# Kernel optimization log

Hardware: AMD Instinct MI355X
Metric: run time of the kernel (lower is better)

The kernel has to match this reference:

```python
import jax, jax.numpy as jnp
import numpy as np

B, T, D = 32, 4096, 256
P, K, L = 2, 17, 3
NH, HD, FF, HID = 8, 32, 2048, 128


def _ln(x, w, b):
    m = x.mean(-1, keepdims=True)
    v = ((x - m) ** 2).mean(-1, keepdims=True)
    return (x - m) * jax.lax.rsqrt(v + 1e-5) * w + b


def _refine(x, w1, b1, w2, b2):
    # x: (B,P,K,D). Vectorized all-pairs: pair[b,p,i,j] = concat(x_i, x_j); MLP; mean over j; residual.
    xi = jnp.broadcast_to(x[:, :, :, None, :], (B, P, K, K, D))
    xj = jnp.broadcast_to(x[:, :, None, :, :], (B, P, K, K, D))
    pair = jnp.concatenate([xi, xj], axis=-1)  # (B,P,K,K,2D)
    h = jax.nn.relu(pair @ w1.T + b1)
    y = (h @ w2.T + b2).mean(axis=3)  # (B,P,K,D)
    return y + x


def _forward(memory, person_q, key_q, sa_in_w, sa_in_b, sa_out_w, sa_out_b,
             ca_in_w, ca_in_b, ca_out_w, ca_out_b, ff1_w, ff1_b, ff2_w, ff2_b,
             ln1_w, ln1_b, ln2_w, ln2_b, ln3_w, ln3_b,
             r1_w1, r1_b1, r1_w2, r1_b2, r2_w1, r2_b1, r2_w2, r2_b2, fc_w, fc_b):
    scale = 1.0 / np.sqrt(HD).astype(np.float32)
    # tgt for person p = person_q[p] + key_q, all persons vectorized into axis P
    x = jnp.broadcast_to(person_q[None, :, None, :] + key_q[None, None, :, :], (B, P, K, D))
    for l in range(L):
        # --- self-attention over K keypoint queries (post-norm TransformerDecoderLayer) ---
        qkv = x @ sa_in_w[l].T + sa_in_b[l]
        q, k, v = jnp.split(qkv, 3, axis=-1)
        qh = q.reshape(B, P, K, NH, HD)
        kh = k.reshape(B, P, K, NH, HD)
        vh = v.reshape(B, P, K, NH, HD)
        a = jax.nn.softmax(jnp.einsum('bpqhd,bpkhd->bphqk', qh, kh) * scale, axis=-1)
        o = jnp.einsum('bphqk,bpkhd->bpqhd', a, vh).reshape(B, P, K, D)
        x = _ln(x + o @ sa_out_w[l].T + sa_out_b[l], ln1_w[l], ln1_b[l])
        # --- cross-attention to memory; memory K/V computed once, shared across persons ---
        q = x @ ca_in_w[l][:D].T + ca_in_b[l][:D]
        mk = memory @ ca_in_w[l][D:2 * D].T + ca_in_b[l][D:2 * D]
        mv = memory @ ca_in_w[l][2 * D:].T + ca_in_b[l][2 * D:]
        qh = q.reshape(B, P, K, NH, HD)
        kh = mk.reshape(B, T, NH, HD)
        vh = mv.reshape(B, T, NH, HD)
        a = jax.nn.softmax(jnp.einsum('bpqhd,bthd->bphqt', qh, kh) * scale, axis=-1)
        o = jnp.einsum('bphqt,bthd->bpqhd', a, vh).reshape(B, P, K, D)
        x = _ln(x + o @ ca_out_w[l].T + ca_out_b[l], ln2_w[l], ln2_b[l])
        # --- feed-forward (ReLU, dim_feedforward=2048 default) ---
        h = jax.nn.relu(x @ ff1_w[l].T + ff1_b[l])
        x = _ln(x + h @ ff2_w[l].T + ff2_b[l], ln3_w[l], ln3_b[l])
    x = _refine(x, r1_w1, r1_b1, r1_w2, r1_b2)
    x = _refine(x, r2_w1, r2_b1, r2_w2, r2_b2)
    return x @ fc_w.T + fc_b  # (B, P, K, 3)


def setup_inputs() -> dict:
    key = jax.random.key(0)
    ks = iter(jax.random.split(key, 48))

    def w(shape, s=0.02):
        return jax.random.normal(next(ks), shape, dtype=jnp.float32) * s

    inp = {
        'memory': jax.random.normal(next(ks), (B, T, D), dtype=jnp.float32),
        'person_q': jax.random.normal(next(ks), (P, D), dtype=jnp.float32),
        'key_q': jax.random.normal(next(ks), (K, D), dtype=jnp.float32),
        'sa_in_w': w((L, 3 * D, D)), 'sa_in_b': jnp.zeros((L, 3 * D)),
        'sa_out_w': w((L, D, D)), 'sa_out_b': jnp.zeros((L, D)),
        'ca_in_w': w((L, 3 * D, D)), 'ca_in_b': jnp.zeros((L, 3 * D)),
        'ca_out_w': w((L, D, D)), 'ca_out_b': jnp.zeros((L, D)),
        'ff1_w': w((L, FF, D)), 'ff1_b': jnp.zeros((L, FF)),
        'ff2_w': w((L, D, FF)), 'ff2_b': jnp.zeros((L, D)),
        'ln1_w': jnp.ones((L, D)), 'ln1_b': jnp.zeros((L, D)),
        'ln2_w': jnp.ones((L, D)), 'ln2_b': jnp.zeros((L, D)),
        'ln3_w': jnp.ones((L, D)), 'ln3_b': jnp.zeros((L, D)),
        'r1_w1': w((HID, 2 * D)), 'r1_b1': jnp.zeros((HID,)),
        'r1_w2': w((D, HID)), 'r1_b2': jnp.zeros((D,)),
        'r2_w1': w((HID, 2 * D)), 'r2_b1': jnp.zeros((HID,)),
        'r2_w2': w((D, HID)), 'r2_b2': jnp.zeros((D,)),
        'fc_w': w((3, D)), 'fc_b': jnp.zeros((3,)),
    }
    return inp


def reference(memory, person_q, key_q, sa_in_w, sa_in_b, sa_out_w, sa_out_b,
              ca_in_w, ca_in_b, ca_out_w, ca_out_b, ff1_w, ff1_b, ff2_w, ff2_b,
              ln1_w, ln1_b, ln2_w, ln2_b, ln3_w, ln3_b,
              r1_w1, r1_b1, r1_w2, r1_b2, r2_w1, r2_b1, r2_w2, r2_b2, fc_w, fc_b):
    return _forward(memory, person_q, key_q, sa_in_w, sa_in_b, sa_out_w, sa_out_b,
                    ca_in_w, ca_in_b, ca_out_w, ca_out_b, ff1_w, ff1_b, ff2_w, ff2_b,
                    ln1_w, ln1_b, ln2_w, ln2_b, ln3_w, ln3_b,
                    r1_w1, r1_b1, r1_w2, r1_b2, r2_w1, r2_b1, r2_w2, r2_b2, fc_w, fc_b)
```

## Files before the change

kernel.cpp:

```cpp
#include <hip/hip_runtime.h>
#include <stdint.h>

#define NB   32
#define TSEQ 4096
#define DD   256
#define PP   2
#define KK   17
#define LL   3
#define NHH  8
#define HDD  32
#define FFD  2048
#define HIDD 128
#define ROWS 1088
#define SCALE 0.17677669529663689f

typedef __attribute__((ext_vector_type(4))) float f32x4;
typedef __attribute__((ext_vector_type(8))) short bf16x8;

static __device__ __forceinline__ unsigned cvtpk(float lo, float hi) {
  unsigned r;
  asm volatile("v_cvt_pk_bf16_f32 %0, %1, %2" : "=v"(r) : "v"(lo), "v"(hi));
  return r;
}
static __device__ __forceinline__ unsigned short f2bf(float f) {
  unsigned int x = __float_as_uint(f);
  return (unsigned short)((x + 0x7fffu + ((x >> 16) & 1u)) >> 16);
}
static __device__ __forceinline__ void gload_lds16(const void* g, void* l) {
  __builtin_amdgcn_global_load_lds(
      (const __attribute__((address_space(1))) unsigned int*)g,
      (__attribute__((address_space(3))) unsigned int*)l, 16, 0, 0);
}

struct CvtJob { const float* src; unsigned short* dst; int n; };
struct CvtJobs8 { CvtJob j[8]; };
__global__ __launch_bounds__(256) void cvt_multi_kernel(CvtJobs8 jobs) {
#pragma unroll
  for (int jj = 0; jj < 8; ++jj) {
    const float* src = jobs.j[jj].src;
    unsigned short* dst = jobs.j[jj].dst;
    const int n8 = jobs.j[jj].n >> 3;
    for (int i = blockIdx.x * 256 + threadIdx.x; i < n8; i += gridDim.x * 256) {
      const float4 f0 = *reinterpret_cast<const float4*>(src + i * 8);
      const float4 f1 = *reinterpret_cast<const float4*>(src + i * 8 + 4);
      uint4 st;
      st.x = cvtpk(f0.x, f0.y); st.y = cvtpk(f0.z, f0.w);
      st.z = cvtpk(f1.x, f1.y); st.w = cvtpk(f1.z, f1.w);
      *reinterpret_cast<uint4*>(dst + i * 8) = st;
    }
  }
}

__global__ __launch_bounds__(256) void init_x_kernel(
    const float* __restrict__ person_q, const float* __restrict__ key_q,
    float* __restrict__ x, unsigned short* __restrict__ x_bf) {
  const int row = blockIdx.x, tid = threadIdx.x;
  const int p = (row / KK) & 1, k = row % KK;
  const float v = person_q[p * DD + tid] + key_q[k * DD + tid];
  x[(size_t)row * DD + tid] = v;
  x_bf[(size_t)row * DD + tid] = f2bf(v);
}

__global__ __launch_bounds__(256) void gemm_kernel(
    const float* __restrict__ X, const float* __restrict__ W,
    const float* __restrict__ bias, const float* __restrict__ R,
    float* __restrict__ Y, int M, int N, int K, int wstride, int relu) {
  __shared__ float As[16][68];
  __shared__ float Bs[16][68];
  const int tid = threadIdx.x;
  const int m0 = blockIdx.y * 64, n0 = blockIdx.x * 64;
  const int tr = tid >> 4, tc = tid & 15;
  const int lr = tid >> 2, lk = (tid & 3) << 2;
  float acc[4][4] = {{0.f, 0.f, 0.f, 0.f}, {0.f, 0.f, 0.f, 0.f},
                     {0.f, 0.f, 0.f, 0.f}, {0.f, 0.f, 0.f, 0.f}};
  for (int k0 = 0; k0 < K; k0 += 16) {
    const float4 av = *reinterpret_cast<const float4*>(&X[(size_t)(m0 + lr) * K + k0 + lk]);
    int wn = n0 + lr; if (wn >= N) wn = N - 1;
    const float4 bv = *reinterpret_cast<const float4*>(&W[(size_t)wn * wstride + k0 + lk]);
    __syncthreads();
    As[lk + 0][lr] = av.x; As[lk + 1][lr] = av.y; As[lk + 2][lr] = av.z; As[lk + 3][lr] = av.w;
    Bs[lk + 0][lr] = bv.x; Bs[lk + 1][lr] = bv.y; Bs[lk + 2][lr] = bv.z; Bs[lk + 3][lr] = bv.w;
    __syncthreads();
#pragma unroll
    for (int kk = 0; kk < 16; ++kk) {
      const float4 a = *reinterpret_cast<const float4*>(&As[kk][tr << 2]);
      const float4 b = *reinterpret_cast<const float4*>(&Bs[kk][tc << 2]);
      const float aa[4] = {a.x, a.y, a.z, a.w};
      const float bb[4] = {b.x, b.y, b.z, b.w};
#pragma unroll
      for (int r = 0; r < 4; ++r)
#pragma unroll
        for (int c = 0; c < 4; ++c) acc[r][c] += aa[r] * bb[c];
    }
  }
#pragma unroll
  for (int r = 0; r < 4; ++r) {
    const int m = m0 + (tr << 2) + r;
#pragma unroll
    for (int c = 0; c < 4; ++c) {
      const int n = n0 + (tc << 2) + c;
      if (n < N) {
        float o = acc[r][c];
        if (bias) o += bias[n];
        if (relu) o = fmaxf(o, 0.f);
        if (R) o += R[(size_t)m * N + n];
        Y[(size_t)m * N + n] = o;
      }
    }
  }
}

__global__ __launch_bounds__(256) void gemm_bf16_kernel(
    const unsigned short* __restrict__ Xbf, const unsigned short* __restrict__ Wbf,
    const float* __restrict__ bias, const float* __restrict__ R,
    float* __restrict__ Yf, unsigned short* __restrict__ Ybf,
    int M, int N, int K, int wstride, int relu) {
  __shared__ unsigned short Xs[64 * 64];
  __shared__ unsigned short Ws[64 * 64];
  const int tid = threadIdx.x, lane = tid & 63, w = tid >> 6;
  const int g = lane >> 4, q16 = lane & 15;
  const int m0 = blockIdx.y * 64, n0 = blockIdx.x * 64;
  f32x4 acc[4];
#pragma unroll
  for (int nt = 0; nt < 4; ++nt) acc[nt] = (f32x4){0.f, 0.f, 0.f, 0.f};

  for (int k0 = 0; k0 < K; k0 += 64) {
    __syncthreads();
#pragma unroll
    for (int j = 0; j < 2; ++j) {
      const int cc = w * 2 + j;
      const int row = cc * 8 + (lane >> 3);
      const int sc = (lane & 7) ^ (row & 7);
      gload_lds16(Xbf + (size_t)(m0 + row) * K + k0 + sc * 8, &Xs[cc * 512]);
      gload_lds16(Wbf + (size_t)(n0 + row) * wstride + k0 + sc * 8, &Ws[cc * 512]);
    }
    asm volatile("s_waitcnt vmcnt(0)" ::: "memory");
    __syncthreads();
    const int arow = w * 16 + q16;
#pragma unroll
    for (int ks = 0; ks < 2; ++ks) {
      const bf16x8 a = *reinterpret_cast<const bf16x8*>(
          &Xs[arow * 64 + ((((ks << 2) + g) ^ (arow & 7)) << 3)]);
#pragma unroll
      for (int nt = 0; nt < 4; ++nt) {
        const int brow = nt * 16 + q16;
        const bf16x8 bfr = *reinterpret_cast<const bf16x8*>(
            &Ws[brow * 64 + ((((ks << 2) + g) ^ (brow & 7)) << 3)]);
        acc[nt] = __builtin_amdgcn_mfma_f32_16x16x32_bf16(a, bfr, acc[nt], 0, 0, 0);
      }
    }
  }
#pragma unroll
  for (int nt = 0; nt < 4; ++nt) {
    const int n = n0 + nt * 16 + q16;
    const float bv = bias ? bias[n] : 0.f;
#pragma unroll
    for (int r = 0; r < 4; ++r) {
      const int m = m0 + w * 16 + g * 4 + r;
      float o = acc[nt][r] + bv;
      if (relu) o = fmaxf(o, 0.f);
      if (R) o += R[(size_t)m * N + n];
      if (Yf) Yf[(size_t)m * N + n] = o;
      if (Ybf) Ybf[(size_t)m * N + n] = f2bf(o);
    }
  }
}

__global__ __launch_bounds__(64) void sa_attn_kernel(
    const float* __restrict__ qkv, unsigned short* __restrict__ attn_bf) {
  const int blk = blockIdx.x;
  const int h = blk & 7, bp = blk >> 3;
  const int rowbase = bp * KK;
  const int tid = threadIdx.x;
  __shared__ float qs[KK][36], ks[KK][36], vs[KK][36];
  __shared__ float ss[KK][20];
  __shared__ float lsum[KK];
  for (int i = tid; i < KK * HDD; i += 64) {
    const int r = i >> 5, d = i & 31;
    const size_t base = (size_t)(rowbase + r) * 768 + h * 32 + d;
    qs[r][d] = qkv[base];
    ks[r][d] = qkv[base + 256];
    vs[r][d] = qkv[base + 512];
  }
  __syncthreads();
  for (int i = tid; i < KK * KK; i += 64) {
    const int q = i / KK, k = i % KK;
    float s = 0.f;
#pragma unroll
    for (int d = 0; d < HDD; ++d) s += qs[q][d] * ks[k][d];
    ss[q][k] = s * SCALE;
  }
  __syncthreads();
  if (tid < KK) {
    float m = -1e30f;
    for (int k = 0; k < KK; ++k) m = fmaxf(m, ss[tid][k]);
    float l = 0.f;
    for (int k = 0; k < KK; ++k) { const float e = __expf(ss[tid][k] - m); ss[tid][k] = e; l += e; }
    lsum[tid] = l;
  }
  __syncthreads();
  for (int i = tid; i < KK * HDD; i += 64) {
    const int q = i >> 5, d = i & 31;
    float o = 0.f;
#pragma unroll
    for (int k = 0; k < KK; ++k) o += ss[q][k] * vs[k][d];
    attn_bf[(size_t)(rowbase + q) * DD + h * 32 + d] = f2bf(o / lsum[q]);
  }
}

__global__ __launch_bounds__(256) void wqk_kernel(
    const float* __restrict__ ca_in_w, unsigned short* __restrict__ Wqk_bf) {
  const int bx = blockIdx.x;
  const int l = bx >> 11, hc = bx & 2047;
  const int h = hc >> 8, c = hc & 255;
  const int d = threadIdx.x;
  const float* Wq = ca_in_w + (size_t)l * 196608 + (size_t)(h * 32) * 256;
  const float* Wk = ca_in_w + (size_t)l * 196608 + (size_t)(256 + h * 32) * 256;
  float acc = 0.f;
#pragma unroll
  for (int j = 0; j < 32; ++j) acc += Wk[(size_t)j * 256 + c] * Wq[(size_t)j * 256 + d];
  Wqk_bf[((size_t)l * 2048 + hc) * 256 + d] = f2bf(acc * SCALE);
}

__global__ __launch_bounds__(256) void bqk_kernel(
    const float* __restrict__ ca_in_w, const float* __restrict__ ca_in_b,
    float* __restrict__ bqk) {
  const int l = blockIdx.x >> 3, h = blockIdx.x & 7;
  const int c = threadIdx.x;
  const float* Wk = ca_in_w + (size_t)l * 196608 + (size_t)(256 + h * 32) * 256;
  const float* bq = ca_in_b + l * 768 + h * 32;
  float acc = 0.f;
#pragma unroll
  for (int j = 0; j < 32; ++j) acc += bq[j] * Wk[(size_t)j * 256 + c];
  bqk[(size_t)l * 2048 + h * 256 + c] = acc * SCALE;
}

__global__ __launch_bounds__(256) void prep_mem_kernel(
    const float* __restrict__ memory, unsigned short* __restrict__ mem_bf,
    unsigned short* __restrict__ memT) {
  const int b = blockIdx.x >> 6, tc = blockIdx.x & 63;
  const int tid = threadIdx.x;
  __shared__ unsigned short tile[64][264];
  for (int it = 0; it < 8; ++it) {
    const int idx = it * 256 + tid;
    const int t = idx >> 5, c8 = (idx & 31) << 3;
    const size_t goff = ((size_t)b * TSEQ + tc * 64 + t) * DD + c8;
    const float4 f0 = *reinterpret_cast<const float4*>(memory + goff);
    const float4 f1 = *reinterpret_cast<const float4*>(memory + goff + 4);
    uint4 st;
    st.x = cvtpk(f0.x, f0.y); st.y = cvtpk(f0.z, f0.w);
    st.z = cvtpk(f1.x, f1.y); st.w = cvtpk(f1.z, f1.w);
    *reinterpret_cast<uint4*>(&tile[t][c8]) = st;
    *reinterpret_cast<uint4*>(mem_bf + goff) = st;
  }
  __syncthreads();
  for (int it = 0; it < 8; ++it) {
    const int idx = it * 256 + tid;
    const int c = idx >> 3, t8 = (idx & 7) << 3;
    union { unsigned short v[8]; uint4 u; } pk;
#pragma unroll
    for (int j = 0; j < 8; ++j) pk.v[j] = tile[t8 + j][c];
    *reinterpret_cast<uint4*>(&memT[((size_t)b * DD + c) * TSEQ + tc * 64 + t8]) = pk.u;
  }
}

#define PS3 72
__global__ __launch_bounds__(256, 2) void ca_fused_kernel(
    const unsigned short* __restrict__ qkeff_bf, const unsigned short* __restrict__ mem_bf,
    const unsigned short* __restrict__ memT,
    float* __restrict__ o_part, float* __restrict__ m_part, float* __restrict__ l_part) {
  const int h = blockIdx.x >> 6;
  const int b = (blockIdx.x >> 1) & 31;
  const int half = blockIdx.x & 1;
  const int tid = threadIdx.x;
  const int lane = tid & 63, w = tid >> 6;
  const int g = lane >> 4, q16 = lane & 15;

  __shared__ unsigned short mem_lds[64 * 256];
  __shared__ unsigned short memT_lds[256 * 64];
  __shared__ unsigned short p_lds[48 * PS3];
  __shared__ float red_m[4 * 48];
  __shared__ float red_l[4 * 48];
  __shared__ float r_lds[48];

  bf16x8 bq[3][8];
#pragma unroll
  for (int qt = 0; qt < 3; ++qt) {
    const int ql = qt * 16 + q16;
    if (ql < 34) {
      const unsigned short* qbase = qkeff_bf + (size_t)(b * 34 + ql) * 2048 + h * 256;
#pragma unroll
      for (int ks = 0; ks < 8; ++ks)
        bq[qt][ks] = *reinterpret_cast<const bf16x8*>(qbase + ks * 32 + g * 8);
    } else {
#pragma unroll
      for (int ks = 0; ks < 8; ++ks) bq[qt][ks] = (bf16x8){0, 0, 0, 0, 0, 0, 0, 0};
    }
  }

  f32x4 ctx[3][4];
#pragma unroll
  for (int mt = 0; mt < 3; ++mt)
#pragma unroll
    for (int nt = 0; nt < 4; ++nt) ctx[mt][nt] = (f32x4){0.f, 0.f, 0.f, 0.f};
  float m_run[3] = {-1e30f, -1e30f, -1e30f};
  float l_run[3] = {0.f, 0.f, 0.f};

  const unsigned short* membb = mem_bf + (size_t)b * TSEQ * DD;
  const unsigned short* memTb = memT + (size_t)b * DD * TSEQ;

  for (int tile = 0; tile < 32; ++tile) {
    const int tbase = half * 2048 + tile * 64;
    __syncthreads();

#pragma unroll
    for (int j = 0; j < 8; ++j) {
      const int cc = w * 8 + j;
      const int trow = cc * 2 + (lane >> 5);
      const int sc = (lane & 31) ^ (trow & 7);
      gload_lds16(membb + (size_t)(tbase + trow) * DD + sc * 8, &mem_lds[cc * 512]);
    }
#pragma unroll
    for (int j = 0; j < 8; ++j) {
      const int cc = w * 8 + j;
      const int crow = cc * 8 + (lane >> 3);
      const int sc = (lane & 7) ^ (crow & 7);
      gload_lds16(memTb + (size_t)crow * TSEQ + tbase + sc * 8, &memT_lds[cc * 512]);
    }
    asm volatile("s_waitcnt vmcnt(0)" ::: "memory");
    __syncthreads();

    f32x4 sacc[3];
#pragma unroll
    for (int qt = 0; qt < 3; ++qt) sacc[qt] = (f32x4){0.f, 0.f, 0.f, 0.f};
    {
      const int arow = w * 16 + q16;
      __builtin_amdgcn_s_setprio(1);
#pragma unroll
      for (int ks = 0; ks < 8; ++ks) {
        const bf16x8 af = *reinterpret_cast<const bf16x8*>(
            &mem_lds[arow * 256 + ((((ks << 2) + g) ^ (arow & 7)) << 3)]);
#pragma unroll
        for (int qt = 0; qt < 3; ++qt)
          sacc[qt] = __builtin_amdgcn_mfma_f32_16x16x32_bf16(af, bq[qt][ks], sacc[qt], 0, 0, 0);
      }
      __builtin_amdgcn_s_setprio(0);
    }

#pragma unroll
    for (int qt = 0; qt < 3; ++qt) {
      float v = fmaxf(fmaxf(sacc[qt][0], sacc[qt][1]), fmaxf(sacc[qt][2], sacc[qt][3]));
      v = fmaxf(v, __shfl_xor(v, 16));
      v = fmaxf(v, __shfl_xor(v, 32));
      if (lane < 16) red_m[w * 48 + qt * 16 + lane] = v;
    }
    __syncthreads();

    float rfac[3], mnew[3];
#pragma unroll
    for (int qt = 0; qt < 3; ++qt) {
      const int q = qt * 16 + q16;
      const float tmax = fmaxf(fmaxf(red_m[q], red_m[48 + q]),
                               fmaxf(red_m[96 + q], red_m[144 + q]));
      mnew[qt] = fmaxf(m_run[qt], tmax);
      rfac[qt] = __expf(m_run[qt] - mnew[qt]);
      m_run[qt] = mnew[qt];
    }
    if (w == 0 && lane < 16) {
#pragma unroll
      for (int qt = 0; qt < 3; ++qt) r_lds[qt * 16 + lane] = rfac[qt];
    }

#pragma unroll
    for (int qt = 0; qt < 3; ++qt) {
      const float p0 = __expf(sacc[qt][0] - mnew[qt]);
      const float p1 = __expf(sacc[qt][1] - mnew[qt]);
      const float p2 = __expf(sacc[qt][2] - mnew[qt]);
      const float p3 = __expf(sacc[qt][3] - mnew[qt]);
      const int prow = (qt * 16 + q16) * PS3 + w * 16 + g * 4;
      *reinterpret_cast<unsigned*>(&p_lds[prow]) = cvtpk(p0, p1);
      *reinterpret_cast<unsigned*>(&p_lds[prow + 2]) = cvtpk(p2, p3);
      float ps = (p0 + p1) + (p2 + p3);
      ps += __shfl_xor(ps, 16);
      ps += __shfl_xor(ps, 32);
      if (lane < 16) red_l[w * 48 + qt * 16 + lane] = ps;
    }
    __syncthreads();

#pragma unroll
    for (int qt = 0; qt < 3; ++qt) {
      const int q = qt * 16 + q16;
      l_run[qt] = l_run[qt] * rfac[qt] +
                  ((red_l[q] + red_l[48 + q]) + (red_l[96 + q] + red_l[144 + q]));
    }
#pragma unroll
    for (int mt = 0; mt < 3; ++mt)
#pragma unroll
      for (int r = 0; r < 4; ++r) {
        const float rr = r_lds[mt * 16 + g * 4 + r];
#pragma unroll
        for (int nt = 0; nt < 4; ++nt) ctx[mt][nt][r] *= rr;
      }

    bf16x8 pf[3][2];
#pragma unroll
    for (int mt = 0; mt < 3; ++mt)
#pragma unroll
      for (int ks2 = 0; ks2 < 2; ++ks2)
        pf[mt][ks2] = *reinterpret_cast<const bf16x8*>(
            &p_lds[(mt * 16 + q16) * PS3 + ks2 * 32 + g * 8]);
    __builtin_amdgcn_s_setprio(1);
#pragma unroll
    for (int nt = 0; nt < 4; ++nt) {
      const int c = w * 64 + nt * 16 + q16;
#pragma unroll
      for (int ks2 = 0; ks2 < 2; ++ks2) {
        const bf16x8 bT = *reinterpret_cast<const bf16x8*>(
            &memT_lds[c * 64 + ((((ks2 << 2) + g) ^ (c & 7)) << 3)]);
#pragma unroll
        for (int mt = 0; mt < 3; ++mt)
          ctx[mt][nt] = __builtin_amdgcn_mfma_f32_16x16x32_bf16(pf[mt][ks2], bT,
                                                                ctx[mt][nt], 0, 0, 0);
      }
    }
    __builtin_amdgcn_s_setprio(0);
  }

#pragma unroll
  for (int mt = 0; mt < 3; ++mt)
#pragma unroll
    for (int r = 0; r < 4; ++r) {
      const int q = mt * 16 + g * 4 + r;
      if (q < 34) {
        const size_t orow = (size_t)(half * ROWS + b * 34 + q) * 2048;
#pragma unroll
        for (int nt = 0; nt < 4; ++nt)
          o_part[orow + h * 256 + w * 64 + nt * 16 + q16] = ctx[mt][nt][r];
      }
    }
  if (w == 0 && lane < 16) {
#pragma unroll
    for (int qt = 0; qt < 3; ++qt) {
      const int q = qt * 16 + lane;
      if (q < 34) {
        const size_t idx = (size_t)(half * ROWS + b * 34 + q) * 8 + h;
        m_part[idx] = m_run[qt];
        l_part[idx] = l_run[qt];
      }
    }
  }
}

__global__ __launch_bounds__(256) void ca_combine_kernel(
    const float* __restrict__ o_part, const float* __restrict__ m_part,
    const float* __restrict__ l_part, unsigned short* __restrict__ ctx_bf) {
  const int row = blockIdx.x, c = threadIdx.x;
#pragma unroll
  for (int h = 0; h < NHH; ++h) {
    const float m0 = m_part[(size_t)row * 8 + h];
    const float m1 = m_part[(size_t)(ROWS + row) * 8 + h];
    const float l0 = l_part[(size_t)row * 8 + h];
    const float l1 = l_part[(size_t)(ROWS + row) * 8 + h];
    const float M = fmaxf(m0, m1);
    const float w0 = __expf(m0 - M), w1 = __expf(m1 - M);
    const float denom = l0 * w0 + l1 * w1;
    const float o0 = o_part[(size_t)row * 2048 + h * 256 + c];
    const float o1 = o_part[(size_t)(ROWS + row) * 2048 + h * 256 + c];
    ctx_bf[(size_t)row * 2048 + h * 256 + c] = f2bf((o0 * w0 + o1 * w1) / denom);
  }
}

__global__ __launch_bounds__(256) void ln_kernel(
    const float* __restrict__ xin, const float* __restrict__ dlt,
    const float* __restrict__ w, const float* __restrict__ b,
    float* __restrict__ xout, unsigned short* __restrict__ xout_bf) {
  const int row = blockIdx.x, tid = threadIdx.x;
  const size_t base = (size_t)row * DD;
  const float v = xin[base + tid] + dlt[base + tid];
  float s = v, s2 = v * v;
#pragma unroll
  for (int off = 32; off > 0; off >>= 1) {
    s += __shfl_down(s, off);
    s2 += __shfl_down(s2, off);
  }
  __shared__ float ps[4], ps2[4];
  if ((tid & 63) == 0) { ps[tid >> 6] = s; ps2[tid >> 6] = s2; }
  __syncthreads();
  const float st = ps[0] + ps[1] + ps[2] + ps[3];
  const float st2 = ps2[0] + ps2[1] + ps2[2] + ps2[3];
  const float mean = st * (1.f / 256.f);
  const float var = st2 * (1.f / 256.f) - mean * mean;
  const float inv = rsqrtf(var + 1e-5f);
  const float o = (v - mean) * inv * w[tid] + b[tid];
  xout[base + tid] = o;
  xout_bf[base + tid] = f2bf(o);
}

__global__ __launch_bounds__(256) void wvo_kernel(
    const float* __restrict__ ca_in_w, const float* __restrict__ ca_out_w,
    unsigned short* __restrict__ Wvo_bf) {
  const int bx = blockIdx.x;
  const int h = bx & 7, dp = (bx >> 3) & 255, l = bx >> 11;
  const int c = threadIdx.x;
  const float* wout = ca_out_w + (size_t)l * 65536 + (size_t)dp * 256 + h * 32;
  const float* wv = ca_in_w + (size_t)l * 196608 + (size_t)(512 + h * 32) * 256 + c;
  float acc = 0.f;
#pragma unroll
  for (int j = 0; j < 32; ++j) acc += wout[j] * wv[(size_t)j * 256];
  Wvo_bf[((size_t)l * 256 + dp) * 2048 + h * 256 + c] = f2bf(acc);
}

__global__ __launch_bounds__(256) void bvo_kernel(
    const float* __restrict__ ca_out_w, const float* __restrict__ ca_in_b,
    const float* __restrict__ ca_out_b, float* __restrict__ bvo) {
  const int l = blockIdx.x, dp = threadIdx.x;
  float acc = ca_out_b[l * 256 + dp];
  for (int j = 0; j < 256; ++j)
    acc += ca_out_w[(size_t)l * 65536 + (size_t)dp * 256 + j] * ca_in_b[l * 768 + 512 + j];
  bvo[l * 256 + dp] = acc;
}

__global__ __launch_bounds__(256) void pairmean_kernel(
    const float* __restrict__ u, const float* __restrict__ v,
    unsigned short* __restrict__ hbar_bf) {
  const int bp = blockIdx.x, tid = threadIdx.x;
  const int r0 = bp * KK;
  __shared__ float us[KK][132], vs[KK][132];
  for (int i = tid; i < KK * HIDD; i += 256) {
    const int r = i >> 7, f = i & 127;
    us[r][f] = u[(size_t)(r0 + r) * HIDD + f];
    vs[r][f] = v[(size_t)(r0 + r) * HIDD + f];
  }
  __syncthreads();
  for (int i = tid; i < KK * HIDD; i += 256) {
    const int r = i >> 7, f = i & 127;
    float s = 0.f;
#pragma unroll
    for (int j = 0; j < KK; ++j) s += fmaxf(us[r][f] + vs[j][f], 0.f);
    hbar_bf[(size_t)(r0 + r) * HIDD + f] = f2bf(s * (1.0f / 17.0f));
  }
}

static void gemm(const float* X, const float* W, const float* bias, const float* R,
                 float* Y, int M, int N, int K, int wstride, int relu, hipStream_t s) {
  dim3 g((N + 63) / 64, M / 64);
  gemm_kernel<<<g, 256, 0, s>>>(X, W, bias, R, Y, M, N, K, wstride, relu);
}
static void gemm_bf(const unsigned short* X, const unsigned short* W, const float* bias,
                    const float* R, float* Yf, unsigned short* Ybf, int M, int N, int K,
                    int wstride, int relu, hipStream_t s) {
  dim3 g(N / 64, M / 64);
  gemm_bf16_kernel<<<g, 256, 0, s>>>(X, W, bias, R, Yf, Ybf, M, N, K, wstride, relu);
}

extern "C" void kernel_launch(void* const* d_in, const int* in_sizes, int n_in,
                              void* d_out, int out_size, void* d_ws, size_t ws_size,
                              hipStream_t stream) {
  const float* memory   = (const float*)d_in[0];
  const float* person_q = (const float*)d_in[1];
  const float* key_q    = (const float*)d_in[2];
  const float* sa_in_w  = (const float*)d_in[3];
  const float* sa_in_b  = (const float*)d_in[4];
  const float* sa_out_w = (const float*)d_in[5];
  const float* sa_out_b = (const float*)d_in[6];
  const float* ca_in_w  = (const float*)d_in[7];
  const float* ca_in_b  = (const float*)d_in[8];
  const float* ca_out_w = (const float*)d_in[9];
  const float* ca_out_b = (const float*)d_in[10];
  const float* ff1_w = (const float*)d_in[11];
  const float* ff1_b = (const float*)d_in[12];
  const float* ff2_w = (const float*)d_in[13];
  const float* ff2_b = (const float*)d_in[14];
  const float* ln1_w = (const float*)d_in[15];
  const float* ln1_b = (const float*)d_in[16];
  const float* ln2_w = (const float*)d_in[17];
  const float* ln2_b = (const float*)d_in[18];
  const float* ln3_w = (const float*)d_in[19];
  const float* ln3_b = (const float*)d_in[20];
  const float* r1_w1 = (const float*)d_in[21];
  const float* r1_b1 = (const float*)d_in[22];
  const float* r1_w2 = (const float*)d_in[23];
  const float* r1_b2 = (const float*)d_in[24];
  const float* r2_w1 = (const float*)d_in[25];
  const float* r2_b1 = (const float*)d_in[26];
  const float* r2_w2 = (const float*)d_in[27];
  const float* r2_b2 = (const float*)d_in[28];
  const float* fc_w  = (const float*)d_in[29];
  const float* fc_b  = (const float*)d_in[30];
  float* out = (float*)d_out;

  char* wsb = (char*)d_ws;
  size_t off = 0;
  auto alloc = [&](size_t bytes) -> char* {
    char* p = wsb + off;
    off += (bytes + 255) & ~(size_t)255;
    return p;
  };
  float* x      = (float*)alloc((size_t)ROWS * DD * 4);
  float* qkv    = (float*)alloc((size_t)ROWS * 768 * 4);
  float* delta  = (float*)alloc((size_t)ROWS * DD * 4);
  float* bvo    = (float*)alloc(3 * 256 * 4);
  float* bqk    = (float*)alloc((size_t)3 * 2048 * 4);
  float* ubuf   = (float*)alloc((size_t)ROWS * HIDD * 4);
  float* vbuf   = (float*)alloc((size_t)ROWS * HIDD * 4);
  float* o_part = (float*)alloc((size_t)2 * ROWS * 2048 * 4);
  float* m_part = (float*)alloc((size_t)2 * ROWS * 8 * 4);
  float* l_part = (float*)alloc((size_t)2 * ROWS * 8 * 4);
  unsigned short* x_bf     = (unsigned short*)alloc((size_t)ROWS * DD * 2);
  unsigned short* attn_bf  = (unsigned short*)alloc((size_t)ROWS * DD * 2);
  unsigned short* hff_bf   = (unsigned short*)alloc((size_t)ROWS * 2048 * 2);
  unsigned short* ctx_bf   = (unsigned short*)alloc((size_t)ROWS * 2048 * 2);
  unsigned short* qkeff_bf = (unsigned short*)alloc((size_t)ROWS * 2048 * 2);
  unsigned short* hbar_bf  = (unsigned short*)alloc((size_t)ROWS * HIDD * 2);
  unsigned short* mem_bf   = (unsigned short*)alloc((size_t)NB * TSEQ * DD * 2);
  unsigned short* memT     = (unsigned short*)alloc((size_t)NB * TSEQ * DD * 2);
  unsigned short* sa_in_bf  = (unsigned short*)alloc((size_t)3 * 768 * 256 * 2);
  unsigned short* sa_out_bf = (unsigned short*)alloc((size_t)3 * 256 * 256 * 2);
  unsigned short* Wqk_bf   = (unsigned short*)alloc((size_t)3 * 2048 * 256 * 2);
  unsigned short* ff1_bf   = (unsigned short*)alloc((size_t)3 * 2048 * 256 * 2);
  unsigned short* ff2_bf   = (unsigned short*)alloc((size_t)3 * 256 * 2048 * 2);
  unsigned short* Wvo_bf   = (unsigned short*)alloc((size_t)3 * 256 * 2048 * 2);
  unsigned short* r1w1_bf  = (unsigned short*)alloc((size_t)HIDD * 512 * 2);
  unsigned short* r1w2_bf  = (unsigned short*)alloc((size_t)DD * HIDD * 2);
  unsigned short* r2w1_bf  = (unsigned short*)alloc((size_t)HIDD * 512 * 2);
  unsigned short* r2w2_bf  = (unsigned short*)alloc((size_t)DD * HIDD * 2);

  prep_mem_kernel<<<NB * 64, 256, 0, stream>>>(memory, mem_bf, memT);
  CvtJobs8 jobs;
  jobs.j[0] = {sa_in_w,  sa_in_bf,  3 * 768 * 256};
  jobs.j[1] = {sa_out_w, sa_out_bf, 3 * 256 * 256};
  jobs.j[2] = {ff1_w,    ff1_bf,    3 * 2048 * 256};
  jobs.j[3] = {ff2_w,    ff2_bf,    3 * 256 * 2048};
  jobs.j[4] = {r1_w1,    r1w1_bf,   HIDD * 512};
  jobs.j[5] = {r1_w2,    r1w2_bf,   DD * HIDD};
  jobs.j[6] = {r2_w1,    r2w1_bf,   HIDD * 512};
  jobs.j[7] = {r2_w2,    r2w2_bf,   DD * HIDD};
  cvt_multi_kernel<<<1024, 256, 0, stream>>>(jobs);
  wqk_kernel<<<6144, 256, 0, stream>>>(ca_in_w, Wqk_bf);
  bqk_kernel<<<24, 256, 0, stream>>>(ca_in_w, ca_in_b, bqk);
  wvo_kernel<<<6144, 256, 0, stream>>>(ca_in_w, ca_out_w, Wvo_bf);
  bvo_kernel<<<3, 256, 0, stream>>>(ca_out_w, ca_in_b, ca_out_b, bvo);
  init_x_kernel<<<ROWS, 256, 0, stream>>>(person_q, key_q, x, x_bf);

  for (int l = 0; l < LL; ++l) {
    gemm_bf(x_bf, sa_in_bf + (size_t)l * 768 * 256, sa_in_b + l * 768, nullptr,
            qkv, nullptr, ROWS, 768, 256, 256, 0, stream);
    sa_attn_kernel<<<512, 64, 0, stream>>>(qkv, attn_bf);
    gemm_bf(attn_bf, sa_out_bf + (size_t)l * 256 * 256, sa_out_b + l * 256, nullptr,
            delta, nullptr, ROWS, 256, 256, 256, 0, stream);
    ln_kernel<<<ROWS, 256, 0, stream>>>(x, delta, ln1_w + l * 256, ln1_b + l * 256, x, x_bf);
    gemm_bf(x_bf, Wqk_bf + (size_t)l * 2048 * 256, bqk + l * 2048, nullptr,
            nullptr, qkeff_bf, ROWS, 2048, 256, 256, 0, stream);
    ca_fused_kernel<<<512, 256, 0, stream>>>(qkeff_bf, mem_bf, memT, o_part, m_part, l_part);
    ca_combine_kernel<<<ROWS, 256, 0, stream>>>(o_part, m_part, l_part, ctx_bf);
    gemm_bf(ctx_bf, Wvo_bf + (size_t)l * 256 * 2048, bvo + l * 256, nullptr,
            delta, nullptr, ROWS, 256, 2048, 2048, 0, stream);
    ln_kernel<<<ROWS, 256, 0, stream>>>(x, delta, ln2_w + l * 256, ln2_b + l * 256, x, x_bf);
    gemm_bf(x_bf, ff1_bf + (size_t)l * 2048 * 256, ff1_b + l * 2048, nullptr,
            nullptr, hff_bf, ROWS, 2048, 256, 256, 1, stream);
    gemm_bf(hff_bf, ff2_bf + (size_t)l * 256 * 2048, ff2_b + l * 256, nullptr,
            delta, nullptr, ROWS, 256, 2048, 2048, 0, stream);
    ln_kernel<<<ROWS, 256, 0, stream>>>(x, delta, ln3_w + l * 256, ln3_b + l * 256, x, x_bf);
  }

  const unsigned short* rw1_bf[2] = {r1w1_bf, r2w1_bf};
  const unsigned short* rw2_bf[2] = {r1w2_bf, r2w2_bf};
  const float* rb1[2] = {r1_b1, r2_b1};
  const float* rb2[2] = {r1_b2, r2_b2};
  for (int r = 0; r < 2; ++r) {
    gemm_bf(x_bf, rw1_bf[r], rb1[r], nullptr, ubuf, nullptr,
            ROWS, 128, 256, 512, 0, stream);
    gemm_bf(x_bf, rw1_bf[r] + 256, nullptr, nullptr, vbuf, nullptr,
            ROWS, 128, 256, 512, 0, stream);
    pairmean_kernel<<<64, 256, 0, stream>>>(ubuf, vbuf, hbar_bf);
    gemm_bf(hbar_bf, rw2_bf[r], rb2[r], x, x, x_bf,
            ROWS, 256, 128, 128, 0, stream);
  }

  gemm(x, fc_w, fc_b, nullptr, out, ROWS, 3, 256, 256, 0, stream);
}
```

Before: 768.8 us.

## Fuse residual add and LayerNorm into full-row bf16 GEMM epilogue; merge prep kernels

Adds a bf16 MFMA GEMM whose block computes 64 full rows of the N=256 output, so the epilogue can add bias and residual and apply LayerNorm in registers. This removes the separate ln_kernel launches and the delta buffer round trip. It also merges the weight-folding and small prep kernels into fewer launches. The cost is that the fused GEMM launches only 17 blocks with K up to 2048, so GPU occupancy is very low for the long-K GEMMs.

```diff
diff --git a/kernel.cpp b/kernel.cpp
--- a/kernel.cpp
+++ b/kernel.cpp
@@ -51,14 +51,34 @@
   }
 }
 
-__global__ __launch_bounds__(256) void init_x_kernel(
+__global__ __launch_bounds__(256) void prep_small_kernel(
     const float* __restrict__ person_q, const float* __restrict__ key_q,
-    float* __restrict__ x, unsigned short* __restrict__ x_bf) {
-  const int row = blockIdx.x, tid = threadIdx.x;
-  const int p = (row / KK) & 1, k = row % KK;
-  const float v = person_q[p * DD + tid] + key_q[k * DD + tid];
-  x[(size_t)row * DD + tid] = v;
-  x_bf[(size_t)row * DD + tid] = f2bf(v);
+    const float* __restrict__ ca_in_w, const float* __restrict__ ca_in_b,
+    const float* __restrict__ ca_out_w, const float* __restrict__ ca_out_b,
+    float* __restrict__ x, unsigned short* __restrict__ x_bf,
+    float* __restrict__ bqk, float* __restrict__ bvo) {
+  const int bx = blockIdx.x, tid = threadIdx.x;
+  if (bx < ROWS) {
+    const int p = (bx / KK) & 1, k = bx % KK;
+    const float v = person_q[p * DD + tid] + key_q[k * DD + tid];
+    x[(size_t)bx * DD + tid] = v;
+    x_bf[(size_t)bx * DD + tid] = f2bf(v);
+  } else if (bx < ROWS + 24) {
+    const int b2 = bx - ROWS;
+    const int l = b2 >> 3, h = b2 & 7;
+    const float* Wk = ca_in_w + (size_t)l * 196608 + (size_t)(256 + h * 32) * 256;
+    const float* bq = ca_in_b + l * 768 + h * 32;
+    float acc = 0.f;
+#pragma unroll
+    for (int j = 0; j < 32; ++j) acc += bq[j] * Wk[(size_t)j * 256 + tid];
+    bqk[(size_t)l * 2048 + h * 256 + tid] = acc * SCALE;
+  } else {
+    const int l = bx - ROWS - 24;
+    float acc = ca_out_b[l * 256 + tid];
+    for (int j = 0; j < 256; ++j)
+      acc += ca_out_w[(size_t)l * 65536 + (size_t)tid * 256 + j] * ca_in_b[l * 768 + 512 + j];
+    bvo[l * 256 + tid] = acc;
+  }
 }
 
 __global__ __launch_bounds__(256) void gemm_kernel(
@@ -166,6 +186,86 @@
   }
 }
 
+__global__ __launch_bounds__(256) void gemm_bf16_ln_kernel(
+    const unsigned short* __restrict__ Xbf, const unsigned short* __restrict__ Wbf,
+    const float* __restrict__ bias, const float* __restrict__ lnw,
+    const float* __restrict__ lnb, float* __restrict__ xio,
+    unsigned short* __restrict__ x_bf, int K, int wstride) {
+  __shared__ unsigned short Xs[64 * 64];
+  __shared__ unsigned short Ws[256 * 64];
+  __shared__ float bias_s[256], lnw_s[256], lnb_s[256];
+  const int tid = threadIdx.x, lane = tid & 63, w = tid >> 6;
+  const int g = lane >> 4, q16 = lane & 15;
+  const int m0 = blockIdx.x * 64;
+  bias_s[tid] = bias[tid];
+  lnw_s[tid] = lnw[tid];
+  lnb_s[tid] = lnb[tid];
+  f32x4 acc[16];
+#pragma unroll
+  for (int nt = 0; nt < 16; ++nt) acc[nt] = (f32x4){0.f, 0.f, 0.f, 0.f};
+
+  for (int k0 = 0; k0 < K; k0 += 64) {
+    __syncthreads();
+#pragma unroll
+    for (int j = 0; j < 2; ++j) {
+      const int cc = w * 2 + j;
+      const int row = cc * 8 + (lane >> 3);
+      const int sc = (lane & 7) ^ (row & 7);
+      gload_lds16(Xbf + (size_t)(m0 + row) * K + k0 + sc * 8, &Xs[cc * 512]);
+    }
+#pragma unroll
+    for (int j = 0; j < 8; ++j) {
+      const int cc = w * 8 + j;
+      const int row = cc * 8 + (lane >> 3);
+      const int sc = (lane & 7) ^ (row & 7);
+      gload_lds16(Wbf + (size_t)row * wstride + k0 + sc * 8, &Ws[cc * 512]);
+    }
+    asm volatile("s_waitcnt vmcnt(0)" ::: "memory");
+    __syncthreads();
+    const int arow = w * 16 + q16;
+#pragma unroll
+    for (int ks = 0; ks < 2; ++ks) {
+      const bf16x8 a = *reinterpret_cast<const bf16x8*>(
+          &Xs[arow * 64 + ((((ks << 2) + g) ^ (arow & 7)) << 3)]);
+#pragma unroll
+      for (int nt = 0; nt < 16; ++nt) {
+        const int brow = nt * 16 + q16;
+        const bf16x8 bfr = *reinterpret_cast<const bf16x8*>(
+            &Ws[brow * 64 + ((((ks << 2) + g) ^ (brow & 7)) << 3)]);
+        acc[nt] = __builtin_amdgcn_mfma_f32_16x16x32_bf16(a, bfr, acc[nt], 0, 0, 0);
+      }
+    }
+  }
+
+#pragma unroll
+  for (int r = 0; r < 4; ++r) {
+    const int m = m0 + w * 16 + g * 4 + r;
+    float s = 0.f, s2 = 0.f;
+#pragma unroll
+    for (int nt = 0; nt < 16; ++nt) {
+      const int n = nt * 16 + q16;
+      const float o = acc[nt][r] + bias_s[n] + xio[(size_t)m * DD + n];
+      acc[nt][r] = o;
+      s += o; s2 += o * o;
+    }
+#pragma unroll
+    for (int off = 1; off < 16; off <<= 1) {
+      s += __shfl_xor(s, off);
+      s2 += __shfl_xor(s2, off);
+    }
+    const float mean = s * (1.f / 256.f);
+    const float var = s2 * (1.f / 256.f) - mean * mean;
+    const float inv = rsqrtf(var + 1e-5f);
+#pragma unroll
+    for (int nt = 0; nt < 16; ++nt) {
+      const int n = nt * 16 + q16;
+      const float v = (acc[nt][r] - mean) * inv * lnw_s[n] + lnb_s[n];
+      xio[(size_t)m * DD + n] = v;
+      x_bf[(size_t)m * DD + n] = f2bf(v);
+    }
+  }
+}
+
 __global__ __launch_bounds__(64) void sa_attn_kernel(
     const float* __restrict__ qkv, unsigned short* __restrict__ attn_bf) {
   const int blk = blockIdx.x;
@@ -208,31 +308,31 @@
   }
 }
 
-__global__ __launch_bounds__(256) void wqk_kernel(
-    const float* __restrict__ ca_in_w, unsigned short* __restrict__ Wqk_bf) {
-  const int bx = blockIdx.x;
-  const int l = bx >> 11, hc = bx & 2047;
-  const int h = hc >> 8, c = hc & 255;
-  const int d = threadIdx.x;
-  const float* Wq = ca_in_w + (size_t)l * 196608 + (size_t)(h * 32) * 256;
-  const float* Wk = ca_in_w + (size_t)l * 196608 + (size_t)(256 + h * 32) * 256;
-  float acc = 0.f;
-#pragma unroll
-  for (int j = 0; j < 32; ++j) acc += Wk[(size_t)j * 256 + c] * Wq[(size_t)j * 256 + d];
-  Wqk_bf[((size_t)l * 2048 + hc) * 256 + d] = f2bf(acc * SCALE);
-}
-
-__global__ __launch_bounds__(256) void bqk_kernel(
-    const float* __restrict__ ca_in_w, const float* __restrict__ ca_in_b,
-    float* __restrict__ bqk) {
-  const int l = blockIdx.x >> 3, h = blockIdx.x & 7;
-  const int c = threadIdx.x;
-  const float* Wk = ca_in_w + (size_t)l * 196608 + (size_t)(256 + h * 32) * 256;
-  const float* bq = ca_in_b + l * 768 + h * 32;
-  float acc = 0.f;
-#pragma unroll
-  for (int j = 0; j < 32; ++j) acc += bq[j] * Wk[(size_t)j * 256 + c];
-  bqk[(size_t)l * 2048 + h * 256 + c] = acc * SCALE;
+__global__ __launch_bounds__(256) void wqkvo_kernel(
+    const float* __restrict__ ca_in_w, const float* __restrict__ ca_out_w,
+    unsigned short* __restrict__ Wqk_bf, unsigned short* __restrict__ Wvo_bf) {
+  const int bx0 = blockIdx.x;
+  if (bx0 < 6144) {
+    const int l = bx0 >> 11, hc = bx0 & 2047;
+    const int h = hc >> 8, c = hc & 255;
+    const int d = threadIdx.x;
+    const float* Wq = ca_in_w + (size_t)l * 196608 + (size_t)(h * 32) * 256;
+    const float* Wk = ca_in_w + (size_t)l * 196608 + (size_t)(256 + h * 32) * 256;
+    float acc = 0.f;
+#pragma unroll
+    for (int j = 0; j < 32; ++j) acc += Wk[(size_t)j * 256 + c] * Wq[(size_t)j * 256 + d];
+    Wqk_bf[((size_t)l * 2048 + hc) * 256 + d] = f2bf(acc * SCALE);
+  } else {
+    const int bx = bx0 - 6144;
+    const int h = bx & 7, dp = (bx >> 3) & 255, l = bx >> 11;
+    const int c = threadIdx.x;
+    const float* wout = ca_out_w + (size_t)l * 65536 + (size_t)dp * 256 + h * 32;
+    const float* wv = ca_in_w + (size_t)l * 196608 + (size_t)(512 + h * 32) * 256 + c;
+    float acc = 0.f;
+#pragma unroll
+    for (int j = 0; j < 32; ++j) acc += wout[j] * wv[(size_t)j * 256];
+    Wvo_bf[((size_t)l * 256 + dp) * 2048 + h * 256 + c] = f2bf(acc);
+  }
 }
 
 __global__ __launch_bounds__(256) void prep_mem_kernel(
@@ -470,56 +570,6 @@
   }
 }
 
-__global__ __launch_bounds__(256) void ln_kernel(
-    const float* __restrict__ xin, const float* __restrict__ dlt,
-    const float* __restrict__ w, const float* __restrict__ b,
-    float* __restrict__ xout, unsigned short* __restrict__ xout_bf) {
-  const int row = blockIdx.x, tid = threadIdx.x;
-  const size_t base = (size_t)row * DD;
-  const float v = xin[base + tid] + dlt[base + tid];
-  float s = v, s2 = v * v;
-#pragma unroll
-  for (int off = 32; off > 0; off >>= 1) {
-    s += __shfl_down(s, off);
-    s2 += __shfl_down(s2, off);
-  }
-  __shared__ float ps[4], ps2[4];
-  if ((tid & 63) == 0) { ps[tid >> 6] = s; ps2[tid >> 6] = s2; }
-  __syncthreads();
-  const float st = ps[0] + ps[1] + ps[2] + ps[3];
-  const float st2 = ps2[0] + ps2[1] + ps2[2] + ps2[3];
-  const float mean = st * (1.f / 256.f);
-  const float var = st2 * (1.f / 256.f) - mean * mean;
-  const float inv = rsqrtf(var + 1e-5f);
-  const float o = (v - mean) * inv * w[tid] + b[tid];
-  xout[base + tid] = o;
-  xout_bf[base + tid] = f2bf(o);
-}
-
-__global__ __launch_bounds__(256) void wvo_kernel(
-    const float* __restrict__ ca_in_w, const float* __restrict__ ca_out_w,
-    unsigned short* __restrict__ Wvo_bf) {
-  const int bx = blockIdx.x;
-  const int h = bx & 7, dp = (bx >> 3) & 255, l = bx >> 11;
-  const int c = threadIdx.x;
-  const float* wout = ca_out_w + (size_t)l * 65536 + (size_t)dp * 256 + h * 32;
-  const float* wv = ca_in_w + (size_t)l * 196608 + (size_t)(512 + h * 32) * 256 + c;
-  float acc = 0.f;
-#pragma unroll
-  for (int j = 0; j < 32; ++j) acc += wout[j] * wv[(size_t)j * 256];
-  Wvo_bf[((size_t)l * 256 + dp) * 2048 + h * 256 + c] = f2bf(acc);
-}
-
-__global__ __launch_bounds__(256) void bvo_kernel(
-    const float* __restrict__ ca_out_w, const float* __restrict__ ca_in_b,
-    const float* __restrict__ ca_out_b, float* __restrict__ bvo) {
-  const int l = blockIdx.x, dp = threadIdx.x;
-  float acc = ca_out_b[l * 256 + dp];
-  for (int j = 0; j < 256; ++j)
-    acc += ca_out_w[(size_t)l * 65536 + (size_t)dp * 256 + j] * ca_in_b[l * 768 + 512 + j];
-  bvo[l * 256 + dp] = acc;
-}
-
 __global__ __launch_bounds__(256) void pairmean_kernel(
     const float* __restrict__ u, const float* __restrict__ v,
     unsigned short* __restrict__ hbar_bf) {
@@ -551,6 +601,11 @@
                     int wstride, int relu, hipStream_t s) {
   dim3 g(N / 64, M / 64);
   gemm_bf16_kernel<<<g, 256, 0, s>>>(X, W, bias, R, Yf, Ybf, M, N, K, wstride, relu);
+}
+static void gemm_ln(const unsigned short* X, const unsigned short* W, const float* bias,
+                    const float* lnw, const float* lnb, float* xio, unsigned short* x_bf,
+                    int K, int wstride, hipStream_t s) {
+  gemm_bf16_ln_kernel<<<ROWS / 64, 256, 0, s>>>(X, W, bias, lnw, lnb, xio, x_bf, K, wstride);
 }
 
 extern "C" void kernel_launch(void* const* d_in, const int* in_sizes, int n_in,
@@ -598,7 +653,6 @@
   };
   float* x      = (float*)alloc((size_t)ROWS * DD * 4);
   float* qkv    = (float*)alloc((size_t)ROWS * 768 * 4);
-  float* delta  = (float*)alloc((size_t)ROWS * DD * 4);
   float* bvo    = (float*)alloc(3 * 256 * 4);
   float* bqk    = (float*)alloc((size_t)3 * 2048 * 4);
   float* ubuf   = (float*)alloc((size_t)ROWS * HIDD * 4);
@@ -636,31 +690,26 @@
   jobs.j[6] = {r2_w1,    r2w1_bf,   HIDD * 512};
   jobs.j[7] = {r2_w2,    r2w2_bf,   DD * HIDD};
   cvt_multi_kernel<<<1024, 256, 0, stream>>>(jobs);
-  wqk_kernel<<<6144, 256, 0, stream>>>(ca_in_w, Wqk_bf);
-  bqk_kernel<<<24, 256, 0, stream>>>(ca_in_w, ca_in_b, bqk);
-  wvo_kernel<<<6144, 256, 0, stream>>>(ca_in_w, ca_out_w, Wvo_bf);
-  bvo_kernel<<<3, 256, 0, stream>>>(ca_out_w, ca_in_b, ca_out_b, bvo);
-  init_x_kernel<<<ROWS, 256, 0, stream>>>(person_q, key_q, x, x_bf);
+  wqkvo_kernel<<<12288, 256, 0, stream>>>(ca_in_w, ca_out_w, Wqk_bf, Wvo_bf);
+  prep_small_kernel<<<ROWS + 24 + 3, 256, 0, stream>>>(
+      person_q, key_q, ca_in_w, ca_in_b, ca_out_w, ca_out_b, x, x_bf, bqk, bvo);
 
   for (int l = 0; l < LL; ++l) {
     gemm_bf(x_bf, sa_in_bf + (size_t)l * 768 * 256, sa_in_b + l * 768, nullptr,
             qkv, nullptr, ROWS, 768, 256, 256, 0, stream);
     sa_attn_kernel<<<512, 64, 0, stream>>>(qkv, attn_bf);
-    gemm_bf(attn_bf, sa_out_bf + (size_t)l * 256 * 256, sa_out_b + l * 256, nullptr,
-            delta, nullptr, ROWS, 256, 256, 256, 0, stream);
-    ln_kernel<<<ROWS, 256, 0, stream>>>(x, delta, ln1_w + l * 256, ln1_b + l * 256, x, x_bf);
+    gemm_ln(attn_bf, sa_out_bf + (size_t)l * 256 * 256, sa_out_b + l * 256,
+            ln1_w + l * 256, ln1_b + l * 256, x, x_bf, 256, 256, stream);
     gemm_bf(x_bf, Wqk_bf + (size_t)l * 2048 * 256, bqk + l * 2048, nullptr,
             nullptr, qkeff_bf, ROWS, 2048, 256, 256, 0, stream);
     ca_fused_kernel<<<512, 256, 0, stream>>>(qkeff_bf, mem_bf, memT, o_part, m_part, l_part);
     ca_combine_kernel<<<ROWS, 256, 0, stream>>>(o_part, m_part, l_part, ctx_bf);
-    gemm_bf(ctx_bf, Wvo_bf + (size_t)l * 256 * 2048, bvo + l * 256, nullptr,
-            delta, nullptr, ROWS, 256, 2048, 2048, 0, stream);
-    ln_kernel<<<ROWS, 256, 0, stream>>>(x, delta, ln2_w + l * 256, ln2_b + l * 256, x, x_bf);
+    gemm_ln(ctx_bf, Wvo_bf + (size_t)l * 256 * 2048, bvo + l * 256,
+            ln2_w + l * 256, ln2_b + l * 256, x, x_bf, 2048, 2048, stream);
     gemm_bf(x_bf, ff1_bf + (size_t)l * 2048 * 256, ff1_b + l * 2048, nullptr,
             nullptr, hff_bf, ROWS, 2048, 256, 256, 1, stream);
-    gemm_bf(hff_bf, ff2_bf + (size_t)l * 256 * 2048, ff2_b + l * 256, nullptr,
-            delta, nullptr, ROWS, 256, 2048, 2048, 0, stream);
-    ln_kernel<<<ROWS, 256, 0, stream>>>(x, delta, ln3_w + l * 256, ln3_b + l * 256, x, x_bf);
+    gemm_ln(hff_bf, ff2_bf + (size_t)l * 256 * 2048, ff2_b + l * 256,
+            ln3_w + l * 256, ln3_b + l * 256, x, x_bf, 2048, 2048, stream);
   }
 
   const unsigned short* rw1_bf[2] = {r1w1_bf, r2w1_bf};
```

New measurement: 897.3 us. +16.7%, slower.
